# Kernel optimization log

Measured on AMD Instinct MI355X. Metric: run time of the kernel, lower is better.

## Reference

```python
import jax, jax.numpy as jnp
import numpy as np

K = 8192
D = 512
BETA = 0.25


def setup_inputs() -> dict:
    key = jax.random.key(0)
    k_z, k_cb = jax.random.split(key)
    z = jax.random.normal(k_z, (8, 4096, D), dtype=jnp.float32)
    codebook = jax.random.normal(k_cb, (K, D), dtype=jnp.float32)
    return {"z": z, "codebook": codebook}


def reference(z, codebook):
    B, Q, Din = z.shape
    flat = z.reshape(-1, Din)                      # (N, D)
    x2 = jnp.sum(flat * flat, axis=1, keepdims=True)   # (N, 1)
    e2 = jnp.sum(codebook * codebook, axis=1)          # (K,)
    xe = flat @ codebook.T                             # (N, K)
    distances = x2 - 2.0 * xe + e2[None, :]
    indices = jnp.argmin(distances, axis=1)            # (N,)
    z_q = codebook[indices].reshape(B, Q, Din)

    codebook_loss = jnp.mean((z_q - jax.lax.stop_gradient(z)) ** 2)
    commitment_loss = jnp.mean((z - jax.lax.stop_gradient(z_q)) ** 2)
    vq_loss = codebook_loss + BETA * commitment_loss
    z_q_ste = z + jax.lax.stop_gradient(z_q - z)

    # perplexity from one-hot usage counts of this batch
    N = flat.shape[0]
    counts = jnp.zeros((codebook.shape[0],), dtype=jnp.float32).at[indices].add(1.0)
    probs = counts / jnp.asarray(N, dtype=jnp.float32)
    perplexity = jnp.exp(-jnp.sum(probs * jnp.log(probs + 1e-10)))

    return z_q_ste, vq_loss, indices.reshape(B, Q), perplexity
```

## Files before the change

kernel.cpp:

```cpp
#include <hip/hip_runtime.h>
#include <hip/hip_bf16.h>

#define K_CODES 8192
#define DIM     512
#define N_VEC   32768
#define MARGIN  0.35f

typedef __attribute__((ext_vector_type(8))) short   short8;
typedef __attribute__((ext_vector_type(8))) unsigned short ushort8;
typedef __attribute__((ext_vector_type(4))) float   float4x;

__device__ inline void gl_lds16(const void* g, void* l) {
    __builtin_amdgcn_global_load_lds(
        (const __attribute__((address_space(1))) unsigned int*)g,
        (__attribute__((address_space(3))) unsigned int*)l, 16, 0, 0);
}

__device__ inline unsigned short f2bf(float f) {
    unsigned int u = __float_as_uint(f);
    return (unsigned short)((u + 0x7FFFu + ((u >> 16) & 1u)) >> 16);
}

__global__ __launch_bounds__(256) void vq_prep(
    const float* __restrict__ z, const float* __restrict__ cb,
    float* __restrict__ x2, float* __restrict__ hne2,
    unsigned short* __restrict__ zh, unsigned short* __restrict__ ch) {
    int wave = threadIdx.x >> 6;
    int lane = threadIdx.x & 63;
    int row  = blockIdx.x * 4 + wave;
    bool isZ = row < N_VEC;
    int lr = isZ ? row : row - N_VEC;
    const float* src = isZ ? z + (size_t)row * DIM : cb + (size_t)lr * DIM;

    const float4* s4 = (const float4*)src;
    float4 v0 = s4[lane * 2];
    float4 v1 = s4[lane * 2 + 1];
    float f[8] = {v0.x, v0.y, v0.z, v0.w, v1.x, v1.y, v1.z, v1.w};

    float s = 0.0f;
    ushort8 h8;
#pragma unroll
    for (int i = 0; i < 8; ++i) { s += f[i] * f[i]; h8[i] = f2bf(f[i]); }
    ((ushort8*)(isZ ? zh : ch))[(size_t)lr * 64 + lane] = h8;

#pragma unroll
    for (int off = 32; off >= 1; off >>= 1) s += __shfl_xor(s, off, 64);
    if (lane == 0) {
        if (isZ) x2[lr] = s;
        else     hne2[lr] = -0.5f * s;
    }
}

__global__ __launch_bounds__(256, 2) void vq_gemm(
    const unsigned short* __restrict__ zh, const unsigned short* __restrict__ ch,
    const float* __restrict__ hne2,
    float* __restrict__ pG, int* __restrict__ pN, float* __restrict__ pG2) {
    __shared__ short8 AsC[1024];
    __shared__ short8 BsC[2048];

    const int tid  = threadIdx.x;
    const int w    = tid >> 6;
    const int lane = tid & 63;
    const int wM   = w & 1;
    const int wN   = w >> 1;
    const int rowBase   = blockIdx.x * 128;
    const int half      = blockIdx.y;
    const int codeBase0 = half * 4096;

    const int low3 = lane & 7, m15 = lane & 15, hi4 = lane >> 4;

    unsigned aOff[4];
#pragma unroll
    for (int i = 0; i < 4; ++i) {
        int cell = (w * 4 + i) * 64 + lane;
        int r = cell >> 3, qs = cell & 7, q = qs ^ (r & 7);
        aOff[i] = ((unsigned)(rowBase + r) * DIM + q * 8) * 2;
    }
    unsigned bOff[8];
#pragma unroll
    for (int i = 0; i < 8; ++i) {
        int cell = (w * 8 + i) * 64 + lane;
        int c = cell >> 3, qs = cell & 7, q = qs ^ (c & 7);
        bOff[i] = ((unsigned)c * DIM + q * 8) * 2;
    }

    int rIdx[4], cIdx[8];
#pragma unroll
    for (int mf = 0; mf < 4; ++mf) rIdx[mf] = (wM * 64 + mf * 16 + m15) * 8;
#pragma unroll
    for (int nf = 0; nf < 8; ++nf) cIdx[nf] = (wN * 128 + nf * 16 + m15) * 8;

    float g1[4][4], g2[4][4];
    int   n1[4][4];
#pragma unroll
    for (int mf = 0; mf < 4; ++mf)
#pragma unroll
        for (int rg = 0; rg < 4; ++rg) {
            g1[mf][rg] = -3.4e38f; g2[mf][rg] = -3.4e38f; n1[mf][rg] = 0;
        }

    const char* pA = (const char*)zh;
    for (int ct = 0; ct < 16; ++ct) {
        const int codeBase = codeBase0 + ct * 256;
        const char* pB = (const char*)ch + (size_t)codeBase * (DIM * 2);
        float4x acc[4][8];
#pragma unroll
        for (int mf = 0; mf < 4; ++mf)
#pragma unroll
            for (int nf = 0; nf < 8; ++nf) acc[mf][nf] = (float4x){0.f, 0.f, 0.f, 0.f};

        for (int dc = 0; dc < DIM; dc += 64) {
            const int dc2 = dc * 2;
            __syncthreads();
#pragma unroll
            for (int i = 0; i < 4; ++i)
                gl_lds16(pA + aOff[i] + dc2, &AsC[(w * 4 + i) * 64]);
#pragma unroll
            for (int i = 0; i < 8; ++i)
                gl_lds16(pB + bOff[i] + dc2, &BsC[(w * 8 + i) * 64]);
            __syncthreads();

#pragma unroll
            for (int ks = 0; ks < 2; ++ks) {
                const int qx = (ks * 4 + hi4) ^ low3;
                short8 a[4];
#pragma unroll
                for (int mf = 0; mf < 4; ++mf) a[mf] = AsC[rIdx[mf] + qx];
#pragma unroll
                for (int nf = 0; nf < 8; ++nf) {
                    short8 b = BsC[cIdx[nf] + qx];
#pragma unroll
                    for (int mf = 0; mf < 4; ++mf)
                        acc[mf][nf] = __builtin_amdgcn_mfma_f32_16x16x32_bf16(
                            a[mf], b, acc[mf][nf], 0, 0, 0);
                }
            }
        }

#pragma unroll
        for (int nf = 0; nf < 8; ++nf) {
            int nb = codeBase + wN * 128 + nf * 16 + m15;
            float hv = hne2[nb];
#pragma unroll
            for (int mf = 0; mf < 4; ++mf) {
#pragma unroll
                for (int rg = 0; rg < 4; ++rg) {
                    float g = acc[mf][nf][rg] + hv;
                    if (g > g1[mf][rg]) {
                        g2[mf][rg] = g1[mf][rg];
                        g1[mf][rg] = g; n1[mf][rg] = nb;
                    } else {
                        g2[mf][rg] = fmaxf(g2[mf][rg], g);
                    }
                }
            }
        }
    }

#pragma unroll
    for (int mf = 0; mf < 4; ++mf)
#pragma unroll
        for (int rg = 0; rg < 4; ++rg) {
            float a1 = g1[mf][rg], a2 = g2[mf][rg];
            int   an = n1[mf][rg];
#pragma unroll
            for (int off = 1; off <= 8; off <<= 1) {
                float b1 = __shfl_xor(a1, off, 64);
                int   bn = __shfl_xor(an, off, 64);
                float b2 = __shfl_xor(a2, off, 64);
                if (b1 > a1 || (b1 == a1 && bn < an)) {
                    a2 = fmaxf(a1, b2); a1 = b1; an = bn;
                } else {
                    a2 = fmaxf(a2, b1);
                }
            }
            if (m15 == 0) {
                int row  = rowBase + wM * 64 + mf * 16 + hi4 * 4 + rg;
                int slot = half * 2 + wN;
                pG [slot * N_VEC + row] = a1;
                pN [slot * N_VEC + row] = an;
                pG2[slot * N_VEC + row] = a2;
            }
        }
}

__global__ __launch_bounds__(256) void vq_scan(
    float* __restrict__ pG, const int* __restrict__ pN,
    const float* __restrict__ pG2,
    int* __restrict__ provIdx, int* __restrict__ flags,
    unsigned long long* __restrict__ keys,
    int* __restrict__ rescueRows, int* __restrict__ rescueCnt) {
    int r = blockIdx.x * 256 + threadIdx.x;
    float g1 = pG[r], g2 = pG2[r];
    int   n1 = pN[r];
#pragma unroll
    for (int s = 1; s < 4; ++s) {
        float a1 = pG [s * N_VEC + r];
        int   an = pN [s * N_VEC + r];
        float a2 = pG2[s * N_VEC + r];
        if (a1 > g1 || (a1 == g1 && an < n1)) {
            g2 = fmaxf(g1, a2); g1 = a1; n1 = an;
        } else {
            g2 = fmaxf(g2, a1);
        }
    }
    provIdx[r] = n1;
    pG[r] = g1;
    int fl = (g1 - g2 < MARGIN) ? 1 : 0;
    flags[r] = fl;
    if (fl) {
        keys[r] = ~0ull;
        int p = atomicAdd(rescueCnt, 1);
        rescueRows[p] = r;
    }
}

#define RBM 64
#define RBK 256
#define RBD 32

__global__ __launch_bounds__(256, 2) void vq_rescue(
    const float* __restrict__ z, const float* __restrict__ cb,
    const float* __restrict__ hne2,
    const int* __restrict__ rescueRows, const int* __restrict__ rescueCnt,
    unsigned long long* __restrict__ keys) {
    __shared__ float As[RBD][RBM];
    __shared__ float Bs[RBD][RBK];
    __shared__ int   rowOf[RBM];

    const int tid = threadIdx.x;
    const int tx  = tid & 31;
    const int ty  = tid >> 5;
    const int cnt = *rescueCnt;
    const int codeBase0 = blockIdx.y * 512;
    const int sw = (tx & 8) ? 4 : 0;
    const int sRow = tid >> 2;
    const int sQ   = tid & 3;

    for (int rt = blockIdx.x; rt * RBM < cnt; rt += gridDim.x) {
        const int slotBase = rt * RBM;
        __syncthreads();
        if (tid < RBM) rowOf[tid] = rescueRows[slotBase + tid];
        __syncthreads();

        float best[8];
        int   bidx[8];
#pragma unroll
        for (int i = 0; i < 8; ++i) { best[i] = 3.4e38f; bidx[i] = K_CODES; }

        for (int kt = 0; kt < 2; ++kt) {
            const int codeBase = codeBase0 + kt * RBK;
            float acc[8][8];
#pragma unroll
            for (int i = 0; i < 8; ++i)
#pragma unroll
                for (int j = 0; j < 8; ++j) acc[i][j] = 0.0f;

            for (int dc = 0; dc < DIM; dc += RBD) {
                __syncthreads();
                {
                    const float* srcA = z + (size_t)rowOf[sRow] * DIM + dc + sQ * 8;
                    float4 va0 = ((const float4*)srcA)[0];
                    float4 va1 = ((const float4*)srcA)[1];
                    int c0 = sQ * 8;
                    As[c0 + 0][sRow] = va0.x; As[c0 + 1][sRow] = va0.y;
                    As[c0 + 2][sRow] = va0.z; As[c0 + 3][sRow] = va0.w;
                    As[c0 + 4][sRow] = va1.x; As[c0 + 5][sRow] = va1.y;
                    As[c0 + 6][sRow] = va1.z; As[c0 + 7][sRow] = va1.w;
                }
                {
                    const float4* srcB = (const float4*)(cb + (size_t)(codeBase + tid) * DIM + dc);
#pragma unroll
                    for (int j = 0; j < 8; ++j) {
                        float4 v = srcB[j];
                        Bs[j * 4 + 0][tid] = v.x; Bs[j * 4 + 1][tid] = v.y;
                        Bs[j * 4 + 2][tid] = v.z; Bs[j * 4 + 3][tid] = v.w;
                    }
                }
                __syncthreads();

#pragma unroll
                for (int d = 0; d < RBD; ++d) {
                    float a[8], b[8];
                    *(float4*)&a[0] = *(const float4*)&As[d][ty * 8];
                    *(float4*)&a[4] = *(const float4*)&As[d][ty * 8 + 4];
                    *(float4*)&b[0] = *(const float4*)&Bs[d][tx * 8 + sw];
                    *(float4*)&b[4] = *(const float4*)&Bs[d][tx * 8 + (sw ^ 4)];
#pragma unroll
                    for (int i = 0; i < 8; ++i)
#pragma unroll
                        for (int j = 0; j < 8; ++j) acc[i][j] += a[i] * b[j];
                }
            }

#pragma unroll
            for (int j = 0; j < 8; ++j) {
                int code = codeBase + tx * 8 + ((j < 4) ? (sw + j) : ((sw ^ 4) + j - 4));
                float ev = -hne2[code];
#pragma unroll
                for (int i = 0; i < 8; ++i) {
                    float kv = ev - acc[i][j];
                    if (kv < best[i] || (kv == best[i] && code < bidx[i])) {
                        best[i] = kv;
                        bidx[i] = code;
                    }
                }
            }
        }

#pragma unroll
        for (int off = 16; off >= 1; off >>= 1) {
#pragma unroll
            for (int i = 0; i < 8; ++i) {
                float od = __shfl_xor(best[i], off, 64);
                int   oi = __shfl_xor(bidx[i], off, 64);
                if (od < best[i] || (od == best[i] && oi < bidx[i])) {
                    best[i] = od;
                    bidx[i] = oi;
                }
            }
        }

        if (tx == 0) {
#pragma unroll
            for (int i = 0; i < 8; ++i) {
                int slot = slotBase + ty * 8 + i;
                if (slot < cnt) {
                    unsigned long long key =
                        ((unsigned long long)__float_as_uint(best[i]) << 32) |
                        (unsigned long long)(unsigned)bidx[i];
                    atomicMin(&keys[rowOf[ty * 8 + i]], key);
                }
            }
        }
    }
}

__global__ __launch_bounds__(256) void vq_final(
    const float* __restrict__ gBest, const int* __restrict__ provIdx,
    const int* __restrict__ flags, const unsigned long long* __restrict__ keys,
    const float* __restrict__ x2, const float* __restrict__ cb,
    float* __restrict__ zq, float* __restrict__ idxf,
    float* __restrict__ counts, float* __restrict__ lossAcc) {
    __shared__ int   sIdx[256];
    __shared__ float wsum[4];
    const int tid = threadIdx.x;
    const int r   = blockIdx.x * 256 + tid;

    int n; float dist;
    if (flags[r]) {
        unsigned long long k = keys[r];
        n = (int)(unsigned)(k & 0xffffffffu);
        float kv = __uint_as_float((unsigned)(k >> 32));
        dist = x2[r] + 2.0f * kv;
    } else {
        n = provIdx[r];
        dist = x2[r] - 2.0f * gBest[r];
    }
    sIdx[tid] = n;
    idxf[r]   = (float)n;
    atomicAdd(&counts[n], 1.0f);

    float ls = dist;
#pragma unroll
    for (int off = 32; off >= 1; off >>= 1) ls += __shfl_xor(ls, off, 64);
    if ((tid & 63) == 0) wsum[tid >> 6] = ls;
    __syncthreads();
    if (tid == 0) atomicAdd(lossAcc, wsum[0] + wsum[1] + wsum[2] + wsum[3]);

    const float4* cb4 = (const float4*)cb;
    float4* zq4 = (float4*)(zq + (size_t)blockIdx.x * 256 * DIM);
    for (int t = tid; t < 256 * (DIM / 4); t += 256) {
        int row = t >> 7, f4 = t & 127;
        zq4[(size_t)row * 128 + f4] = cb4[(size_t)sIdx[row] * 128 + f4];
    }
}

__global__ __launch_bounds__(256) void vq_finalize(const float* __restrict__ counts,
                                                   const float* __restrict__ lossAcc,
                                                   float* __restrict__ out_loss,
                                                   float* __restrict__ out_perp) {
    __shared__ float wsum[4];
    int tid = threadIdx.x;
    float s = 0.0f;
    for (int i = tid; i < K_CODES; i += 256) {
        float p = counts[i] * (1.0f / (float)N_VEC);
        s += p * logf(p + 1e-10f);
    }
#pragma unroll
    for (int off = 32; off >= 1; off >>= 1) s += __shfl_xor(s, off, 64);
    if ((tid & 63) == 0) wsum[tid >> 6] = s;
    __syncthreads();
    if (tid == 0) {
        *out_perp = expf(-(wsum[0] + wsum[1] + wsum[2] + wsum[3]));
        *out_loss = 1.25f * lossAcc[0] / (float)(N_VEC * DIM);
    }
}

extern "C" void kernel_launch(void* const* d_in, const int* in_sizes, int n_in,
                              void* d_out, int out_size, void* d_ws, size_t ws_size,
                              hipStream_t stream) {
    (void)in_sizes; (void)n_in; (void)out_size; (void)ws_size;
    const float* z  = (const float*)d_in[0];
    const float* cb = (const float*)d_in[1];

    char* ws = (char*)d_ws;
    float* x2        = (float*)(ws + 0);
    float* hne2      = (float*)(ws + 131072);
    float* counts    = (float*)(ws + 163840);
    float* lossAcc   = (float*)(ws + 196608);
    int*   rescueCnt = (int*)  (ws + 196612);
    int*   provIdx   = (int*)  (ws + 262144);
    int*   flags     = (int*)  (ws + 393216);
    unsigned long long* keys = (unsigned long long*)(ws + 524288);
    int*   rescueRows = (int*) (ws + 786432);
    float* pG        = (float*)(ws + 1048576);
    int*   pN        = (int*)  (ws + 1572864);
    float* pG2       = (float*)(ws + 2097152);
    unsigned short* zh = (unsigned short*)(ws + 2621440);
    unsigned short* ch = (unsigned short*)(ws + 36175872);

    float* out      = (float*)d_out;
    float* zq       = out;
    float* out_loss = out + 16777216;
    float* idxf     = out + 16777217;
    float* out_perp = out + 16777217 + 32768;

    hipMemsetAsync(counts, 0, 32768 + 8, stream);
    hipMemsetAsync(rescueRows, 0, 131072, stream);
    vq_prep<<<(N_VEC + K_CODES) / 4, 256, 0, stream>>>(z, cb, x2, hne2, zh, ch);
    dim3 grid(N_VEC / 128, 2);
    vq_gemm<<<grid, 256, 0, stream>>>(zh, ch, hne2, pG, pN, pG2);
    vq_scan<<<N_VEC / 256, 256, 0, stream>>>(pG, pN, pG2, provIdx, flags, keys,
                                             rescueRows, rescueCnt);
    dim3 rgrid(64, 16);
    vq_rescue<<<rgrid, 256, 0, stream>>>(z, cb, hne2, rescueRows, rescueCnt, keys);
    vq_final<<<N_VEC / 256, 256, 0, stream>>>(pG, provIdx, flags, keys, x2, cb,
                                              zq, idxf, counts, lossAcc);
    vq_finalize<<<1, 256, 0, stream>>>(counts, lossAcc, out_loss, out_perp);
}
```

Measured before the change: 657.6 us.

## Track top-2 candidates in bf16 GEMM and resolve two-way ties cheaply

The bf16 GEMM epilogue now keeps the best two code indices plus a third-best score per row, instead of only the best index and the second score. The scan sends rows whose third candidate is also close to the full fp32 rescue path. Rows with only one close rival go to a new lightweight kernel that recomputes the two fp32 dot products exactly. This is meant to shrink the costly rescue GEMM, at the price of more epilogue registers, extra shuffles in the GEMM, and scratch buffers placed in the output area before it is overwritten.

```diff
diff --git a/kernel.cpp b/kernel.cpp
--- a/kernel.cpp
+++ b/kernel.cpp
@@ -54,7 +54,8 @@
 __global__ __launch_bounds__(256, 2) void vq_gemm(
     const unsigned short* __restrict__ zh, const unsigned short* __restrict__ ch,
     const float* __restrict__ hne2,
-    float* __restrict__ pG, int* __restrict__ pN, float* __restrict__ pG2) {
+    float* __restrict__ pG, int* __restrict__ pN, float* __restrict__ pG2,
+    int* __restrict__ pN2, float* __restrict__ pG3) {
     __shared__ short8 AsC[1024];
     __shared__ short8 BsC[2048];
 
@@ -90,13 +91,14 @@
 #pragma unroll
     for (int nf = 0; nf < 8; ++nf) cIdx[nf] = (wN * 128 + nf * 16 + m15) * 8;
 
-    float g1[4][4], g2[4][4];
-    int   n1[4][4];
+    float g1v[4][4], g2v[4][4], g3v[4][4];
+    unsigned nn[4][4];
 #pragma unroll
     for (int mf = 0; mf < 4; ++mf)
 #pragma unroll
         for (int rg = 0; rg < 4; ++rg) {
-            g1[mf][rg] = -3.4e38f; g2[mf][rg] = -3.4e38f; n1[mf][rg] = 0;
+            g1v[mf][rg] = -3.4e38f; g2v[mf][rg] = -3.4e38f;
+            g3v[mf][rg] = -3.4e38f; nn[mf][rg] = 0u;
         }
 
     const char* pA = (const char*)zh;
@@ -146,12 +148,14 @@
 #pragma unroll
                 for (int rg = 0; rg < 4; ++rg) {
                     float g = acc[mf][nf][rg] + hv;
-                    if (g > g1[mf][rg]) {
-                        g2[mf][rg] = g1[mf][rg];
-                        g1[mf][rg] = g; n1[mf][rg] = nb;
-                    } else {
-                        g2[mf][rg] = fmaxf(g2[mf][rg], g);
-                    }
+                    bool t1 = g > g1v[mf][rg];
+                    bool t2 = g > g2v[mf][rg];
+                    g3v[mf][rg] = t2 ? g2v[mf][rg] : fmaxf(g3v[mf][rg], g);
+                    unsigned nup = t1 ? ((nn[mf][rg] << 16) | (unsigned)nb)
+                                      : (((unsigned)nb << 16) | (nn[mf][rg] & 0xFFFFu));
+                    nn[mf][rg]  = t2 ? nup : nn[mf][rg];
+                    g2v[mf][rg] = t1 ? g1v[mf][rg] : (t2 ? g : g2v[mf][rg]);
+                    g1v[mf][rg] = t1 ? g : g1v[mf][rg];
                 }
             }
         }
@@ -161,57 +165,125 @@
     for (int mf = 0; mf < 4; ++mf)
 #pragma unroll
         for (int rg = 0; rg < 4; ++rg) {
-            float a1 = g1[mf][rg], a2 = g2[mf][rg];
-            int   an = n1[mf][rg];
+            float a1 = g1v[mf][rg], a2 = g2v[mf][rg], a3 = g3v[mf][rg];
+            int an1 = (int)(nn[mf][rg] & 0xFFFFu);
+            int an2 = (int)(nn[mf][rg] >> 16);
 #pragma unroll
             for (int off = 1; off <= 8; off <<= 1) {
                 float b1 = __shfl_xor(a1, off, 64);
-                int   bn = __shfl_xor(an, off, 64);
                 float b2 = __shfl_xor(a2, off, 64);
-                if (b1 > a1 || (b1 == a1 && bn < an)) {
-                    a2 = fmaxf(a1, b2); a1 = b1; an = bn;
-                } else {
-                    a2 = fmaxf(a2, b1);
-                }
+                float b3 = __shfl_xor(a3, off, 64);
+                int  bn1 = __shfl_xor(an1, off, 64);
+                int  bn2 = __shfl_xor(an2, off, 64);
+                if (b1 > a1 || (b1 == a1 && bn1 < an1)) {
+                    a3 = a2; a2 = a1; an2 = an1; a1 = b1; an1 = bn1;
+                } else if (b1 > a2 || (b1 == a2 && bn1 < an2)) {
+                    a3 = a2; a2 = b1; an2 = bn1;
+                } else a3 = fmaxf(a3, b1);
+                if (b2 > a1 || (b2 == a1 && bn2 < an1)) {
+                    a3 = a2; a2 = a1; an2 = an1; a1 = b2; an1 = bn2;
+                } else if (b2 > a2 || (b2 == a2 && bn2 < an2)) {
+                    a3 = a2; a2 = b2; an2 = bn2;
+                } else a3 = fmaxf(a3, b2);
+                a3 = fmaxf(a3, b3);
             }
             if (m15 == 0) {
                 int row  = rowBase + wM * 64 + mf * 16 + hi4 * 4 + rg;
                 int slot = half * 2 + wN;
                 pG [slot * N_VEC + row] = a1;
-                pN [slot * N_VEC + row] = an;
+                pN [slot * N_VEC + row] = an1;
                 pG2[slot * N_VEC + row] = a2;
+                pN2[slot * N_VEC + row] = an2;
+                pG3[slot * N_VEC + row] = a3;
             }
         }
 }
 
 __global__ __launch_bounds__(256) void vq_scan(
     float* __restrict__ pG, const int* __restrict__ pN,
-    const float* __restrict__ pG2,
+    const float* __restrict__ pG2, const int* __restrict__ pN2,
+    const float* __restrict__ pG3,
     int* __restrict__ provIdx, int* __restrict__ flags,
     unsigned long long* __restrict__ keys,
-    int* __restrict__ rescueRows, int* __restrict__ rescueCnt) {
+    int* __restrict__ rescueRows, int* __restrict__ rescueCnt,
+    int* __restrict__ pairRows, int* __restrict__ pairCnt,
+    int* __restrict__ mergedN2) {
     int r = blockIdx.x * 256 + threadIdx.x;
-    float g1 = pG[r], g2 = pG2[r];
-    int   n1 = pN[r];
+    float g1 = pG[r], g2 = pG2[r], g3 = pG3[r];
+    int   n1 = pN[r], n2 = pN2[r];
 #pragma unroll
     for (int s = 1; s < 4; ++s) {
         float a1 = pG [s * N_VEC + r];
-        int   an = pN [s * N_VEC + r];
+        int  an1 = pN [s * N_VEC + r];
         float a2 = pG2[s * N_VEC + r];
-        if (a1 > g1 || (a1 == g1 && an < n1)) {
-            g2 = fmaxf(g1, a2); g1 = a1; n1 = an;
-        } else {
-            g2 = fmaxf(g2, a1);
-        }
+        int  an2 = pN2[s * N_VEC + r];
+        float a3 = pG3[s * N_VEC + r];
+        if (a1 > g1 || (a1 == g1 && an1 < n1)) {
+            g3 = g2; g2 = g1; n2 = n1; g1 = a1; n1 = an1;
+        } else if (a1 > g2 || (a1 == g2 && an1 < n2)) {
+            g3 = g2; g2 = a1; n2 = an1;
+        } else g3 = fmaxf(g3, a1);
+        if (a2 > g1 || (a2 == g1 && an2 < n1)) {
+            g3 = g2; g2 = g1; n2 = n1; g1 = a2; n1 = an2;
+        } else if (a2 > g2 || (a2 == g2 && an2 < n2)) {
+            g3 = g2; g2 = a2; n2 = an2;
+        } else g3 = fmaxf(g3, a2);
+        g3 = fmaxf(g3, a3);
     }
     provIdx[r] = n1;
     pG[r] = g1;
-    int fl = (g1 - g2 < MARGIN) ? 1 : 0;
-    flags[r] = fl;
-    if (fl) {
-        keys[r] = ~0ull;
+    int fl = 0;
+    if (g1 - g3 < MARGIN) {
+        fl = 1; keys[r] = ~0ull;
         int p = atomicAdd(rescueCnt, 1);
         rescueRows[p] = r;
+    } else if (g1 - g2 < MARGIN) {
+        fl = 1; keys[r] = ~0ull;
+        mergedN2[r] = n2;
+        int p = atomicAdd(pairCnt, 1);
+        pairRows[p] = r;
+    }
+    flags[r] = fl;
+}
+
+__global__ __launch_bounds__(256) void vq_pair(
+    const float* __restrict__ z, const float* __restrict__ cb,
+    const float* __restrict__ hne2,
+    const int* __restrict__ provIdx, const int* __restrict__ mergedN2,
+    const int* __restrict__ pairRows, const int* __restrict__ pairCnt,
+    unsigned long long* __restrict__ keys) {
+    const int lane = threadIdx.x & 63;
+    const int wid  = blockIdx.x * 4 + (threadIdx.x >> 6);
+    const int nW   = gridDim.x * 4;
+    const int cnt  = *pairCnt;
+    for (int i = wid; i < cnt; i += nW) {
+        int r  = pairRows[i];
+        int n1 = provIdx[r];
+        int n2 = mergedN2[r];
+        const float4* xz = (const float4*)(z  + (size_t)r  * DIM);
+        const float4* c1 = (const float4*)(cb + (size_t)n1 * DIM);
+        const float4* c2 = (const float4*)(cb + (size_t)n2 * DIM);
+        float4 x0 = xz[lane * 2], x1 = xz[lane * 2 + 1];
+        float4 a0 = c1[lane * 2], a1 = c1[lane * 2 + 1];
+        float4 b0 = c2[lane * 2], b1 = c2[lane * 2 + 1];
+        float d1 = x0.x*a0.x + x0.y*a0.y + x0.z*a0.z + x0.w*a0.w
+                 + x1.x*a1.x + x1.y*a1.y + x1.z*a1.z + x1.w*a1.w;
+        float d2 = x0.x*b0.x + x0.y*b0.y + x0.z*b0.z + x0.w*b0.w
+                 + x1.x*b1.x + x1.y*b1.y + x1.z*b1.z + x1.w*b1.w;
+#pragma unroll
+        for (int off = 32; off >= 1; off >>= 1) {
+            d1 += __shfl_xor(d1, off, 64);
+            d2 += __shfl_xor(d2, off, 64);
+        }
+        if (lane == 0) {
+            float kv1 = -hne2[n1] - d1;
+            float kv2 = -hne2[n2] - d2;
+            int nsel; float kv;
+            if (kv2 < kv1 || (kv2 == kv1 && n2 < n1)) { kv = kv2; nsel = n2; }
+            else                                      { kv = kv1; nsel = n1; }
+            keys[r] = ((unsigned long long)__float_as_uint(kv) << 32) |
+                      (unsigned long long)(unsigned)nsel;
+        }
     }
 }
 
@@ -410,6 +482,7 @@
     float* counts    = (float*)(ws + 163840);
     float* lossAcc   = (float*)(ws + 196608);
     int*   rescueCnt = (int*)  (ws + 196612);
+    int*   pairCnt   = (int*)  (ws + 196616);
     int*   provIdx   = (int*)  (ws + 262144);
     int*   flags     = (int*)  (ws + 393216);
     unsigned long long* keys = (unsigned long long*)(ws + 524288);
@@ -426,13 +499,22 @@
     float* idxf     = out + 16777217;
     float* out_perp = out + 16777217 + 32768;
 
-    hipMemsetAsync(counts, 0, 32768 + 8, stream);
+    char* sc = (char*)d_out;
+    int*   pN2      = (int*)  (sc + 0);
+    float* pG3      = (float*)(sc + 524288);
+    int*   mergedN2 = (int*)  (sc + 1048576);
+    int*   pairRows = (int*)  (sc + 1179648);
+
+    hipMemsetAsync(counts, 0, 32768 + 16, stream);
     hipMemsetAsync(rescueRows, 0, 131072, stream);
     vq_prep<<<(N_VEC + K_CODES) / 4, 256, 0, stream>>>(z, cb, x2, hne2, zh, ch);
     dim3 grid(N_VEC / 128, 2);
-    vq_gemm<<<grid, 256, 0, stream>>>(zh, ch, hne2, pG, pN, pG2);
-    vq_scan<<<N_VEC / 256, 256, 0, stream>>>(pG, pN, pG2, provIdx, flags, keys,
-                                             rescueRows, rescueCnt);
+    vq_gemm<<<grid, 256, 0, stream>>>(zh, ch, hne2, pG, pN, pG2, pN2, pG3);
+    vq_scan<<<N_VEC / 256, 256, 0, stream>>>(pG, pN, pG2, pN2, pG3, provIdx, flags,
+                                             keys, rescueRows, rescueCnt,
+                                             pairRows, pairCnt, mergedN2);
+    vq_pair<<<128, 256, 0, stream>>>(z, cb, hne2, provIdx, mergedN2,
+                                     pairRows, pairCnt, keys);
     dim3 rgrid(64, 16);
     vq_rescue<<<rgrid, 256, 0, stream>>>(z, cb, hne2, rescueRows, rescueCnt, keys);
     vq_final<<<N_VEC / 256, 256, 0, stream>>>(pG, provIdx, flags, keys, x2, cb,
```

Measured after the change: 738.3 us. 1.12x slower.

## Pack code index into float mantissa, shrink GEMM tile, split codes into quarters

Applied to the files above, without the earlier changes.

The bf16 MFMA GEMM tile shrinks from 128x256 to 128x128 with a four-way split of the codebook, so LDS use is smaller and the launch bound allows three blocks per CU. The per-thread top-2 tracking becomes branchless: a 10-bit index tag is packed into the low mantissa bits of each score, and fmax/fmed3 update best and second best without a separate index register. The scan kernel decodes the index from the tag, and partial results go to scratch space in the output buffer. The rescue margin is widened to absorb the mantissa truncation, at the cost of more rows sent to the fp32 rescue pass, whose tiling is reworked to one 256-code tile per block.

```diff
diff --git a/kernel.cpp b/kernel.cpp
--- a/kernel.cpp
+++ b/kernel.cpp
@@ -4,7 +4,7 @@
 #define K_CODES 8192
 #define DIM     512
 #define N_VEC   32768
-#define MARGIN  0.35f
+#define MARGIN  0.5f
 
 typedef __attribute__((ext_vector_type(8))) short   short8;
 typedef __attribute__((ext_vector_type(8))) unsigned short ushort8;
@@ -19,6 +19,10 @@
 __device__ inline unsigned short f2bf(float f) {
     unsigned int u = __float_as_uint(f);
     return (unsigned short)((u + 0x7FFFu + ((u >> 16) & 1u)) >> 16);
+}
+
+__device__ inline float med3(float a, float b, float c) {
+    return __builtin_amdgcn_fmed3f(a, b, c);
 }
 
 __global__ __launch_bounds__(256) void vq_prep(
@@ -51,63 +55,54 @@
     }
 }
 
-__global__ __launch_bounds__(256, 2) void vq_gemm(
+__global__ __launch_bounds__(256, 3) void vq_gemm(
     const unsigned short* __restrict__ zh, const unsigned short* __restrict__ ch,
     const float* __restrict__ hne2,
-    float* __restrict__ pG, int* __restrict__ pN, float* __restrict__ pG2) {
+    float* __restrict__ pP1, float* __restrict__ pP2) {
     __shared__ short8 AsC[1024];
-    __shared__ short8 BsC[2048];
+    __shared__ short8 BsC[1024];
 
     const int tid  = threadIdx.x;
     const int w    = tid >> 6;
     const int lane = tid & 63;
-    const int wM   = w & 1;
-    const int wN   = w >> 1;
+    const int wM   = w >> 1;
+    const int wN   = w & 1;
     const int rowBase   = blockIdx.x * 128;
-    const int half      = blockIdx.y;
-    const int codeBase0 = half * 4096;
+    const int quarter   = blockIdx.y;
+    const int codeBase0 = quarter * 2048;
 
     const int low3 = lane & 7, m15 = lane & 15, hi4 = lane >> 4;
 
-    unsigned aOff[4];
+    unsigned aOff[4], bOff[4];
 #pragma unroll
     for (int i = 0; i < 4; ++i) {
         int cell = (w * 4 + i) * 64 + lane;
         int r = cell >> 3, qs = cell & 7, q = qs ^ (r & 7);
         aOff[i] = ((unsigned)(rowBase + r) * DIM + q * 8) * 2;
-    }
-    unsigned bOff[8];
-#pragma unroll
-    for (int i = 0; i < 8; ++i) {
-        int cell = (w * 8 + i) * 64 + lane;
-        int c = cell >> 3, qs = cell & 7, q = qs ^ (c & 7);
-        bOff[i] = ((unsigned)c * DIM + q * 8) * 2;
-    }
-
-    int rIdx[4], cIdx[8];
+        bOff[i] = ((unsigned)r * DIM + q * 8) * 2;
+    }
+
+    int rIdx[4], cIdx[4];
 #pragma unroll
     for (int mf = 0; mf < 4; ++mf) rIdx[mf] = (wM * 64 + mf * 16 + m15) * 8;
 #pragma unroll
-    for (int nf = 0; nf < 8; ++nf) cIdx[nf] = (wN * 128 + nf * 16 + m15) * 8;
-
-    float g1[4][4], g2[4][4];
-    int   n1[4][4];
+    for (int nf = 0; nf < 4; ++nf) cIdx[nf] = (wN * 64 + nf * 16 + m15) * 8;
+
+    float p1[4][4], p2[4][4];
 #pragma unroll
     for (int mf = 0; mf < 4; ++mf)
 #pragma unroll
-        for (int rg = 0; rg < 4; ++rg) {
-            g1[mf][rg] = -3.4e38f; g2[mf][rg] = -3.4e38f; n1[mf][rg] = 0;
-        }
+        for (int rg = 0; rg < 4; ++rg) { p1[mf][rg] = -3.4e38f; p2[mf][rg] = -3.4e38f; }
 
     const char* pA = (const char*)zh;
     for (int ct = 0; ct < 16; ++ct) {
-        const int codeBase = codeBase0 + ct * 256;
+        const int codeBase = codeBase0 + ct * 128;
         const char* pB = (const char*)ch + (size_t)codeBase * (DIM * 2);
-        float4x acc[4][8];
+        float4x acc[4][4];
 #pragma unroll
         for (int mf = 0; mf < 4; ++mf)
 #pragma unroll
-            for (int nf = 0; nf < 8; ++nf) acc[mf][nf] = (float4x){0.f, 0.f, 0.f, 0.f};
+            for (int nf = 0; nf < 4; ++nf) acc[mf][nf] = (float4x){0.f, 0.f, 0.f, 0.f};
 
         for (int dc = 0; dc < DIM; dc += 64) {
             const int dc2 = dc * 2;
@@ -116,96 +111,89 @@
             for (int i = 0; i < 4; ++i)
                 gl_lds16(pA + aOff[i] + dc2, &AsC[(w * 4 + i) * 64]);
 #pragma unroll
-            for (int i = 0; i < 8; ++i)
-                gl_lds16(pB + bOff[i] + dc2, &BsC[(w * 8 + i) * 64]);
+            for (int i = 0; i < 4; ++i)
+                gl_lds16(pB + bOff[i] + dc2, &BsC[(w * 4 + i) * 64]);
             __syncthreads();
 
 #pragma unroll
             for (int ks = 0; ks < 2; ++ks) {
                 const int qx = (ks * 4 + hi4) ^ low3;
-                short8 a[4];
+                short8 a[4], b[4];
 #pragma unroll
                 for (int mf = 0; mf < 4; ++mf) a[mf] = AsC[rIdx[mf] + qx];
 #pragma unroll
-                for (int nf = 0; nf < 8; ++nf) {
-                    short8 b = BsC[cIdx[nf] + qx];
+                for (int nf = 0; nf < 4; ++nf) b[nf] = BsC[cIdx[nf] + qx];
+#pragma unroll
+                for (int nf = 0; nf < 4; ++nf)
 #pragma unroll
                     for (int mf = 0; mf < 4; ++mf)
                         acc[mf][nf] = __builtin_amdgcn_mfma_f32_16x16x32_bf16(
-                            a[mf], b, acc[mf][nf], 0, 0, 0);
+                            a[mf], b[nf], acc[mf][nf], 0, 0, 0);
+            }
+        }
+
+#pragma unroll
+        for (int nf = 0; nf < 4; ++nf) {
+            int nb = codeBase + wN * 64 + nf * 16 + m15;
+            float hv = hne2[nb];
+            unsigned tag = ((unsigned)ct << 6) | ((unsigned)nf << 4) | (unsigned)m15;
+#pragma unroll
+            for (int mf = 0; mf < 4; ++mf) {
+#pragma unroll
+                for (int rg = 0; rg < 4; ++rg) {
+                    float g  = acc[mf][nf][rg] + hv;
+                    float pk = __uint_as_float(
+                        (__float_as_uint(g) & 0xFFFFFC00u) | tag);
+                    p2[mf][rg] = med3(pk, p1[mf][rg], p2[mf][rg]);
+                    p1[mf][rg] = fmaxf(p1[mf][rg], pk);
                 }
             }
         }
-
-#pragma unroll
-        for (int nf = 0; nf < 8; ++nf) {
-            int nb = codeBase + wN * 128 + nf * 16 + m15;
-            float hv = hne2[nb];
-#pragma unroll
-            for (int mf = 0; mf < 4; ++mf) {
-#pragma unroll
-                for (int rg = 0; rg < 4; ++rg) {
-                    float g = acc[mf][nf][rg] + hv;
-                    if (g > g1[mf][rg]) {
-                        g2[mf][rg] = g1[mf][rg];
-                        g1[mf][rg] = g; n1[mf][rg] = nb;
-                    } else {
-                        g2[mf][rg] = fmaxf(g2[mf][rg], g);
-                    }
-                }
-            }
-        }
     }
 
 #pragma unroll
     for (int mf = 0; mf < 4; ++mf)
 #pragma unroll
         for (int rg = 0; rg < 4; ++rg) {
-            float a1 = g1[mf][rg], a2 = g2[mf][rg];
-            int   an = n1[mf][rg];
+            float a1 = p1[mf][rg], a2 = p2[mf][rg];
 #pragma unroll
             for (int off = 1; off <= 8; off <<= 1) {
                 float b1 = __shfl_xor(a1, off, 64);
-                int   bn = __shfl_xor(an, off, 64);
                 float b2 = __shfl_xor(a2, off, 64);
-                if (b1 > a1 || (b1 == a1 && bn < an)) {
-                    a2 = fmaxf(a1, b2); a1 = b1; an = bn;
-                } else {
-                    a2 = fmaxf(a2, b1);
-                }
+                a2 = med3(b1, a1, a2);
+                a1 = fmaxf(a1, b1);
+                a2 = med3(b2, a1, a2);
             }
             if (m15 == 0) {
                 int row  = rowBase + wM * 64 + mf * 16 + hi4 * 4 + rg;
-                int slot = half * 2 + wN;
-                pG [slot * N_VEC + row] = a1;
-                pN [slot * N_VEC + row] = an;
-                pG2[slot * N_VEC + row] = a2;
+                int slot = quarter * 2 + wN;
+                pP1[(size_t)slot * N_VEC + row] = a1;
+                pP2[(size_t)slot * N_VEC + row] = a2;
             }
         }
 }
 
 __global__ __launch_bounds__(256) void vq_scan(
-    float* __restrict__ pG, const int* __restrict__ pN,
-    const float* __restrict__ pG2,
-    int* __restrict__ provIdx, int* __restrict__ flags,
+    const float* __restrict__ pP1, const float* __restrict__ pP2,
+    float* __restrict__ pG, int* __restrict__ provIdx, int* __restrict__ flags,
     unsigned long long* __restrict__ keys,
     int* __restrict__ rescueRows, int* __restrict__ rescueCnt) {
     int r = blockIdx.x * 256 + threadIdx.x;
-    float g1 = pG[r], g2 = pG2[r];
-    int   n1 = pN[r];
-#pragma unroll
-    for (int s = 1; s < 4; ++s) {
-        float a1 = pG [s * N_VEC + r];
-        int   an = pN [s * N_VEC + r];
-        float a2 = pG2[s * N_VEC + r];
-        if (a1 > g1 || (a1 == g1 && an < n1)) {
-            g2 = fmaxf(g1, a2); g1 = a1; n1 = an;
-        } else {
-            g2 = fmaxf(g2, a1);
-        }
-    }
+    float g1 = -3.4e38f, g2 = -3.4e38f;
+    int   s1v = 0;
+#pragma unroll
+    for (int s = 0; s < 8; ++s) {
+        float a1 = pP1[(size_t)s * N_VEC + r];
+        float a2 = pP2[(size_t)s * N_VEC + r];
+        if (a1 > g1)      { g2 = g1; g1 = a1; s1v = s; }
+        else if (a1 > g2) { g2 = a1; }
+        if (a2 > g2)      { g2 = a2; }
+    }
+    unsigned u1 = __float_as_uint(g1);
+    int t  = (int)(u1 & 0x3FFu);
+    int n1 = (s1v >> 1) * 2048 + (s1v & 1) * 64 + ((t >> 6) * 128) + (t & 63);
     provIdx[r] = n1;
-    pG[r] = g1;
+    pG[r] = __uint_as_float(u1 & 0xFFFFFC00u);
     int fl = (g1 - g2 < MARGIN) ? 1 : 0;
     flags[r] = fl;
     if (fl) {
@@ -232,8 +220,7 @@
     const int tx  = tid & 31;
     const int ty  = tid >> 5;
     const int cnt = *rescueCnt;
-    const int codeBase0 = blockIdx.y * 512;
-    const int sw = (tx & 8) ? 4 : 0;
+    const int codeBase = blockIdx.y * RBK;
     const int sRow = tid >> 2;
     const int sQ   = tid & 3;
 
@@ -243,67 +230,64 @@
         if (tid < RBM) rowOf[tid] = rescueRows[slotBase + tid];
         __syncthreads();
 
+        float acc[8][8];
+#pragma unroll
+        for (int i = 0; i < 8; ++i)
+#pragma unroll
+            for (int j = 0; j < 8; ++j) acc[i][j] = 0.0f;
+
+        for (int dc = 0; dc < DIM; dc += RBD) {
+            __syncthreads();
+            {
+                const float* srcA = z + (size_t)rowOf[sRow] * DIM + dc + sQ * 8;
+                float4 va0 = ((const float4*)srcA)[0];
+                float4 va1 = ((const float4*)srcA)[1];
+                int c0 = sQ * 8;
+                As[c0 + 0][sRow] = va0.x; As[c0 + 1][sRow] = va0.y;
+                As[c0 + 2][sRow] = va0.z; As[c0 + 3][sRow] = va0.w;
+                As[c0 + 4][sRow] = va1.x; As[c0 + 5][sRow] = va1.y;
+                As[c0 + 6][sRow] = va1.z; As[c0 + 7][sRow] = va1.w;
+            }
+            {
+                const float4* srcB = (const float4*)(cb + (size_t)(codeBase + tid) * DIM + dc);
+#pragma unroll
+                for (int j = 0; j < 8; ++j) {
+                    float4 v = srcB[j];
+                    Bs[j * 4 + 0][tid] = v.x; Bs[j * 4 + 1][tid] = v.y;
+                    Bs[j * 4 + 2][tid] = v.z; Bs[j * 4 + 3][tid] = v.w;
+                }
+            }
+            __syncthreads();
+
+#pragma unroll
+            for (int d = 0; d < RBD; ++d) {
+                float a[8], b[8];
+                *(float4*)&a[0] = *(const float4*)&As[d][ty * 8];
+                *(float4*)&a[4] = *(const float4*)&As[d][ty * 8 + 4];
+#pragma unroll
+                for (int j = 0; j < 8; ++j) b[j] = Bs[d][tx + 32 * j];
+#pragma unroll
+                for (int i = 0; i < 8; ++i)
+#pragma unroll
+                    for (int j = 0; j < 8; ++j) acc[i][j] += a[i] * b[j];
+            }
+        }
+
         float best[8];
         int   bidx[8];
 #pragma unroll
         for (int i = 0; i < 8; ++i) { best[i] = 3.4e38f; bidx[i] = K_CODES; }
 
-        for (int kt = 0; kt < 2; ++kt) {
-            const int codeBase = codeBase0 + kt * RBK;
-            float acc[8][8];
-#pragma unroll
-            for (int i = 0; i < 8; ++i)
-#pragma unroll
-                for (int j = 0; j < 8; ++j) acc[i][j] = 0.0f;
-
-            for (int dc = 0; dc < DIM; dc += RBD) {
-                __syncthreads();
-                {
-                    const float* srcA = z + (size_t)rowOf[sRow] * DIM + dc + sQ * 8;
-                    float4 va0 = ((const float4*)srcA)[0];
-                    float4 va1 = ((const float4*)srcA)[1];
-                    int c0 = sQ * 8;
-                    As[c0 + 0][sRow] = va0.x; As[c0 + 1][sRow] = va0.y;
-                    As[c0 + 2][sRow] = va0.z; As[c0 + 3][sRow] = va0.w;
-                    As[c0 + 4][sRow] = va1.x; As[c0 + 5][sRow] = va1.y;
-                    As[c0 + 6][sRow] = va1.z; As[c0 + 7][sRow] = va1.w;
-                }
-                {
-                    const float4* srcB = (const float4*)(cb + (size_t)(codeBase + tid) * DIM + dc);
-#pragma unroll
-                    for (int j = 0; j < 8; ++j) {
-                        float4 v = srcB[j];
-                        Bs[j * 4 + 0][tid] = v.x; Bs[j * 4 + 1][tid] = v.y;
-                        Bs[j * 4 + 2][tid] = v.z; Bs[j * 4 + 3][tid] = v.w;
-                    }
-                }
-                __syncthreads();
-
-#pragma unroll
-                for (int d = 0; d < RBD; ++d) {
-                    float a[8], b[8];
-                    *(float4*)&a[0] = *(const float4*)&As[d][ty * 8];
-                    *(float4*)&a[4] = *(const float4*)&As[d][ty * 8 + 4];
-                    *(float4*)&b[0] = *(const float4*)&Bs[d][tx * 8 + sw];
-                    *(float4*)&b[4] = *(const float4*)&Bs[d][tx * 8 + (sw ^ 4)];
-#pragma unroll
-                    for (int i = 0; i < 8; ++i)
-#pragma unroll
-                        for (int j = 0; j < 8; ++j) acc[i][j] += a[i] * b[j];
-                }
-            }
-
-#pragma unroll
-            for (int j = 0; j < 8; ++j) {
-                int code = codeBase + tx * 8 + ((j < 4) ? (sw + j) : ((sw ^ 4) + j - 4));
-                float ev = -hne2[code];
-#pragma unroll
-                for (int i = 0; i < 8; ++i) {
-                    float kv = ev - acc[i][j];
-                    if (kv < best[i] || (kv == best[i] && code < bidx[i])) {
-                        best[i] = kv;
-                        bidx[i] = code;
-                    }
+#pragma unroll
+        for (int j = 0; j < 8; ++j) {
+            int code = codeBase + tx + 32 * j;
+            float ev = -hne2[code];
+#pragma unroll
+            for (int i = 0; i < 8; ++i) {
+                float kv = ev - acc[i][j];
+                if (kv < best[i] || (kv == best[i] && code < bidx[i])) {
+                    best[i] = kv;
+                    bidx[i] = code;
                 }
             }
         }
@@ -415,8 +399,6 @@
     unsigned long long* keys = (unsigned long long*)(ws + 524288);
     int*   rescueRows = (int*) (ws + 786432);
     float* pG        = (float*)(ws + 1048576);
-    int*   pN        = (int*)  (ws + 1572864);
-    float* pG2       = (float*)(ws + 2097152);
     unsigned short* zh = (unsigned short*)(ws + 2621440);
     unsigned short* ch = (unsigned short*)(ws + 36175872);
 
@@ -426,14 +408,18 @@
     float* idxf     = out + 16777217;
     float* out_perp = out + 16777217 + 32768;
 
+    char* sc = (char*)d_out;
+    float* pP1 = (float*)(sc + 0);
+    float* pP2 = (float*)(sc + 1048576);
+
     hipMemsetAsync(counts, 0, 32768 + 8, stream);
     hipMemsetAsync(rescueRows, 0, 131072, stream);
     vq_prep<<<(N_VEC + K_CODES) / 4, 256, 0, stream>>>(z, cb, x2, hne2, zh, ch);
-    dim3 grid(N_VEC / 128, 2);
-    vq_gemm<<<grid, 256, 0, stream>>>(zh, ch, hne2, pG, pN, pG2);
-    vq_scan<<<N_VEC / 256, 256, 0, stream>>>(pG, pN, pG2, provIdx, flags, keys,
+    dim3 grid(N_VEC / 128, 4);
+    vq_gemm<<<grid, 256, 0, stream>>>(zh, ch, hne2, pP1, pP2);
+    vq_scan<<<N_VEC / 256, 256, 0, stream>>>(pP1, pP2, pG, provIdx, flags, keys,
                                              rescueRows, rescueCnt);
-    dim3 rgrid(64, 16);
+    dim3 rgrid(32, 32);
     vq_rescue<<<rgrid, 256, 0, stream>>>(z, cb, hne2, rescueRows, rescueCnt, keys);
     vq_final<<<N_VEC / 256, 256, 0, stream>>>(pG, provIdx, flags, keys, x2, cb,
                                               zq, idxf, counts, lossAcc);
```

New measurement: 1.235 ms. +87.7%, slower.
